# Optimization experiments

Measured on AMD Instinct MI355X. Metric: run time of the kernel, lower is better.

## Reference

```python
import jax, jax.numpy as jnp
import numpy as np

# Dimensions
N = 100000      # nodes
E = 500000      # edges
D_IN = 128      # in_channels
H, C = 2, 64    # heads, out_channels per head (out_channels=128)
T = 128         # time_enc.out_channels
MSG = 128       # msg_dim
EDGE_DIM = MSG + T  # 256
SCALE = 1.0 / np.sqrt(C)


def setup_inputs() -> dict:
    key = jax.random.key(0)
    ks = jax.random.split(key, 16)
    s = 0.05
    x = jax.random.normal(ks[0], (N, D_IN), dtype=jnp.float32)
    last_update = jax.random.uniform(ks[1], (N,), dtype=jnp.float32)
    edge_index = jax.random.randint(ks[2], (2, E), 0, N, dtype=jnp.int64)
    t = jax.random.uniform(ks[3], (E,), dtype=jnp.float32) + 1.0  # event times >= last_update typically
    msg = jax.random.normal(ks[4], (E, MSG), dtype=jnp.float32)
    # TimeEncoder: cos(Linear(1, T))
    time_w = jax.random.normal(ks[5], (T, 1), dtype=jnp.float32) * s
    time_b = jax.random.normal(ks[6], (T,), dtype=jnp.float32) * s
    # TransformerConv linear layers (PyG defaults: q/k/v with bias, edge without, skip with bias)
    Wq = jax.random.normal(ks[7], (D_IN, H * C), dtype=jnp.float32) * s
    bq = jnp.zeros((H * C,), dtype=jnp.float32)
    Wk = jax.random.normal(ks[8], (D_IN, H * C), dtype=jnp.float32) * s
    bk = jnp.zeros((H * C,), dtype=jnp.float32)
    Wv = jax.random.normal(ks[9], (D_IN, H * C), dtype=jnp.float32) * s
    bv = jnp.zeros((H * C,), dtype=jnp.float32)
    We = jax.random.normal(ks[10], (EDGE_DIM, H * C), dtype=jnp.float32) * s
    Wskip = jax.random.normal(ks[11], (D_IN, H * C), dtype=jnp.float32) * s
    bskip = jnp.zeros((H * C,), dtype=jnp.float32)
    return dict(x=x, last_update=last_update, edge_index=edge_index, t=t, msg=msg,
                time_w=time_w, time_b=time_b, Wq=Wq, bq=bq, Wk=Wk, bk=bk,
                Wv=Wv, bv=bv, We=We, Wskip=Wskip, bskip=bskip)


def reference(x, last_update, edge_index, t, msg, time_w, time_b,
              Wq, bq, Wk, bk, Wv, bv, We, Wskip, bskip):
    src, dst = edge_index[0], edge_index[1]
    # relative time encoding: cos(Linear(1, T)(rel_t))
    rel_t = t - last_update[src]                                   # [E]
    rel_t_enc = jnp.cos(rel_t[:, None] * time_w[:, 0][None, :] + time_b)  # [E, T]
    edge_attr = jnp.concatenate([rel_t_enc, msg], axis=-1)         # [E, EDGE_DIM]

    # TransformerConv (heads=H, per-head dim C, eval mode so no dropout)
    q = (x @ Wq + bq).reshape(N, H, C)
    k = (x @ Wk + bk).reshape(N, H, C)
    v = (x @ Wv + bv).reshape(N, H, C)
    e = (edge_attr @ We).reshape(E, H, C)

    k_j = k[src] + e                                               # [E, H, C]
    logits = jnp.sum(q[dst] * k_j, axis=-1) * SCALE                # [E, H]

    # segment softmax over destination nodes
    m = jax.ops.segment_max(logits, dst, num_segments=N)           # [N, H]
    p = jnp.exp(logits - m[dst])
    denom = jax.ops.segment_sum(p, dst, num_segments=N)
    alpha = p / (denom[dst] + 1e-16)                               # [E, H]

    msgs = (v[src] + e) * alpha[..., None]                         # [E, H, C]
    out = jax.ops.segment_sum(msgs, dst, num_segments=N).reshape(N, H * C)
    # root/skip connection
    return out + x @ Wskip + bskip
```

## Files before the change

### kernel.cpp

```cpp
#include <hip/hip_runtime.h>
#include <hip/hip_bf16.h>
#include <math.h>


#define SCALE_ATTN 0.125f
#define SCAN_CHUNK 512

typedef __attribute__((ext_vector_type(8))) short bf16x8;
typedef __attribute__((ext_vector_type(4))) float f32x4;

union AFrag { bf16x8 v; unsigned int w[4]; unsigned short u[8]; };

__device__ __forceinline__ unsigned short f2bf(float f) {
    __hip_bfloat16 h = __float2bfloat16(f);
    unsigned short u;
    __builtin_memcpy(&u, &h, 2);
    return u;
}
__device__ __forceinline__ unsigned int f2bf2(float lo, float hi) {
    __hip_bfloat162 h2 = __float22bfloat162_rn(float2{lo, hi});
    unsigned int u;
    __builtin_memcpy(&u, &h2, 4);
    return u;
}
__device__ __forceinline__ float bf2f(unsigned int lo16) {
    return __uint_as_float(lo16 << 16);
}
__device__ __forceinline__ void unpack8(uint4 u, float* f) {
    f[0] = bf2f(u.x & 0xffffu); f[1] = bf2f(u.x >> 16);
    f[2] = bf2f(u.y & 0xffffu); f[3] = bf2f(u.y >> 16);
    f[4] = bf2f(u.z & 0xffffu); f[5] = bf2f(u.z >> 16);
    f[6] = bf2f(u.w & 0xffffu); f[7] = bf2f(u.w >> 16);
}
__device__ __forceinline__ bf16x8 pack2(float4 a, float4 b) {
    AFrag f;
    f.w[0] = f2bf2(a.x, a.y);
    f.w[1] = f2bf2(a.z, a.w);
    f.w[2] = f2bf2(b.x, b.y);
    f.w[3] = f2bf2(b.z, b.w);
    return f.v;
}

__global__ __launch_bounds__(256) void k_zero(int4* __restrict__ p, int n4)
{
    const int i = blockIdx.x * 256 + threadIdx.x;
    if (i < n4) p[i] = make_int4(0, 0, 0, 0);
}

__global__ __launch_bounds__(512, 4) void k_node_mfma(
    const float4* __restrict__ x4,
    const float* __restrict__ Wq, const float* __restrict__ Wk,
    const float* __restrict__ Wv, const float* __restrict__ Ws,
    const float* __restrict__ bq, const float* __restrict__ bk,
    const float* __restrict__ bv, const float* __restrict__ bs,
    unsigned short* __restrict__ qb, unsigned short* __restrict__ kb,
    unsigned short* __restrict__ vb, unsigned short* __restrict__ skb,
    int N, int numTiles)
{
    __shared__ __align__(16) unsigned short sX[32 * 128];
    const int tid = threadIdx.x;
    const int w = tid >> 6, l = tid & 63;
    const int l15 = l & 15, lg = l >> 4;
    const int mat = w >> 1;
    const int colbase = (w & 1) * 64;

    const float* Wm = (mat == 0) ? Wq : (mat == 1) ? Wk : (mat == 2) ? Wv : Ws;
    const float* bm = (mat == 0) ? bq : (mat == 1) ? bk : (mat == 2) ? bv : bs;
    unsigned short* dst = (mat == 0) ? qb : (mat == 1) ? kb : (mat == 2) ? vb : skb;

    bf16x8 Bf[4][4];
    float bias[4];
    #pragma unroll
    for (int nt = 0; nt < 4; ++nt) {
        const int col = colbase + nt * 16 + l15;
        bias[nt] = bm[col];
        #pragma unroll
        for (int ks = 0; ks < 4; ++ks) {
            AFrag f;
            #pragma unroll
            for (int j = 0; j < 4; ++j)
                f.w[j] = f2bf2(Wm[(ks * 32 + lg * 8 + j * 2) * 128 + col],
                               Wm[(ks * 32 + lg * 8 + j * 2 + 1) * 128 + col]);
            Bf[ks][nt] = f.v;
        }
    }

    for (int tile = blockIdx.x; tile < numTiles; tile += gridDim.x) {
        {
            const int e = tid >> 4, k8 = tid & 15;
            const int row = min(tile * 32 + e, N - 1);
            const float4 a0 = x4[(size_t)row * 32 + k8 * 2];
            const float4 a1 = x4[(size_t)row * 32 + k8 * 2 + 1];
            const int byteoff = (e * 256 + k8 * 16) ^ ((e & 7) << 4);
            *(bf16x8*)((char*)sX + byteoff) = pack2(a0, a1);
        }
        __syncthreads();

        f32x4 acc[2][4];
        #pragma unroll
        for (int m = 0; m < 2; ++m)
            #pragma unroll
            for (int nt = 0; nt < 4; ++nt) acc[m][nt] = (f32x4)(0.f);

        #pragma unroll
        for (int m = 0; m < 2; ++m) {
            const int lrow = m * 16 + l15;
            #pragma unroll
            for (int ks = 0; ks < 4; ++ks) {
                const int byteoff = (lrow * 256 + ks * 64 + lg * 16) ^ ((lrow & 7) << 4);
                const bf16x8 a = *(const bf16x8*)((const char*)sX + byteoff);
                #pragma unroll
                for (int nt = 0; nt < 4; ++nt)
                    acc[m][nt] = __builtin_amdgcn_mfma_f32_16x16x32_bf16(a, Bf[ks][nt], acc[m][nt], 0, 0, 0);
            }
        }

        #pragma unroll
        for (int m = 0; m < 2; ++m) {
            #pragma unroll
            for (int nt = 0; nt < 4; ++nt) {
                const int col = colbase + nt * 16 + l15;
                #pragma unroll
                for (int r = 0; r < 4; ++r) {
                    const int node = tile * 32 + m * 16 + lg * 4 + r;
                    if (node < N)
                        dst[(size_t)node * 128 + col] = f2bf(acc[m][nt][r] + bias[nt]);
                }
            }
        }
        __syncthreads();
    }
}

__global__ __launch_bounds__(256, 2) void k_edge_mfma(
    const float4* __restrict__ msg4,
    const float* __restrict__ relo,
    const float4* __restrict__ tw4, const float4* __restrict__ tb4,
    const float* __restrict__ We,
    unsigned short* __restrict__ ebuf, int E, int numTiles)
{
    __shared__ __align__(16) unsigned short sWe[128 * 256];
    __shared__ __align__(16) unsigned short sMsg[64 * 128];
    const int tid = threadIdx.x;
    const int w = tid >> 6, l = tid & 63;
    const int l15 = l & 15, lg = l >> 4;
    const int ch = w & 1;
    const int mp = w >> 1;

    for (int c = tid; c < 4096; c += 256) {
        const int n = c >> 5, k0 = (c & 31) << 3;
        AFrag af;
        #pragma unroll
        for (int j = 0; j < 4; ++j)
            af.w[j] = f2bf2(We[(k0 + j * 2) * 128 + n], We[(k0 + j * 2 + 1) * 128 + n]);
        const int byteoff = ((n << 9) + (k0 << 1)) ^ ((n & 7) << 4);
        *(bf16x8*)((char*)sWe + byteoff) = af.v;
    }
    __syncthreads();

    for (int tile = blockIdx.x; tile < numTiles; tile += gridDim.x) {
        const int ebase = tile * 64;

        #pragma unroll
        for (int i = 0; i < 4; ++i) {
            const int U = tid + i * 256;
            const int e = U >> 4, u = U & 15;
            const int er = min(ebase + e, E - 1);
            const float4 a0 = msg4[(size_t)er * 32 + u * 2];
            const float4 a1 = msg4[(size_t)er * 32 + u * 2 + 1];
            const int byteoff = (e << 8) + ((u ^ (e & 7)) << 4);
            *(bf16x8*)((char*)sMsg + byteoff) = pack2(a0, a1);
        }
        __syncthreads();

        const int r0 = mp * 32 + l15;
        const int r1 = r0 + 16;
        const float rel0 = relo[min(ebase + r0, E - 1)];
        const float rel1 = relo[min(ebase + r1, E - 1)];

        f32x4 acc0[4], acc1[4];
        #pragma unroll
        for (int i = 0; i < 4; ++i) { acc0[i] = (f32x4)(0.f); acc1[i] = (f32x4)(0.f); }

        #pragma unroll
        for (int kk = 0; kk < 4; ++kk) {
            const int kbase = (kk << 5) + (lg << 3);

            const float4 tww = tw4[kbase >> 2];
            const float4 tw2 = tw4[(kbase >> 2) + 1];
            const float4 tbb = tb4[kbase >> 2];
            const float4 tb2 = tb4[(kbase >> 2) + 1];
            AFrag a0, a1;
            a0.w[0] = f2bf2(__cosf(fmaf(rel0, tww.x, tbb.x)),
                            __cosf(fmaf(rel0, tww.y, tbb.y)));
            a0.w[1] = f2bf2(__cosf(fmaf(rel0, tww.z, tbb.z)),
                            __cosf(fmaf(rel0, tww.w, tbb.w)));
            a0.w[2] = f2bf2(__cosf(fmaf(rel0, tw2.x, tb2.x)),
                            __cosf(fmaf(rel0, tw2.y, tb2.y)));
            a0.w[3] = f2bf2(__cosf(fmaf(rel0, tw2.z, tb2.z)),
                            __cosf(fmaf(rel0, tw2.w, tb2.w)));
            a1.w[0] = f2bf2(__cosf(fmaf(rel1, tww.x, tbb.x)),
                            __cosf(fmaf(rel1, tww.y, tbb.y)));
            a1.w[1] = f2bf2(__cosf(fmaf(rel1, tww.z, tbb.z)),
                            __cosf(fmaf(rel1, tww.w, tbb.w)));
            a1.w[2] = f2bf2(__cosf(fmaf(rel1, tw2.x, tb2.x)),
                            __cosf(fmaf(rel1, tw2.y, tb2.y)));
            a1.w[3] = f2bf2(__cosf(fmaf(rel1, tw2.z, tb2.z)),
                            __cosf(fmaf(rel1, tw2.w, tb2.w)));

            const int mu = (kk << 2) + lg;
            const bf16x8 am0 = *(const bf16x8*)((const char*)sMsg +
                                 ((r0 << 8) + ((mu ^ (r0 & 7)) << 4)));
            const bf16x8 am1 = *(const bf16x8*)((const char*)sMsg +
                                 ((r1 << 8) + ((mu ^ (r1 & 7)) << 4)));

            #pragma unroll
            for (int nt = 0; nt < 4; ++nt) {
                const int nrow = ch * 64 + nt * 16 + l15;
                const int swz = (nrow & 7) << 4;
                const bf16x8 bC = *(const bf16x8*)((const char*)sWe +
                                   (((nrow << 9) + (kbase << 1)) ^ swz));
                acc0[nt] = __builtin_amdgcn_mfma_f32_16x16x32_bf16(a0.v, bC, acc0[nt], 0, 0, 0);
                acc1[nt] = __builtin_amdgcn_mfma_f32_16x16x32_bf16(a1.v, bC, acc1[nt], 0, 0, 0);
                const bf16x8 bM = *(const bf16x8*)((const char*)sWe +
                                   (((nrow << 9) + ((128 + kbase) << 1)) ^ swz));
                acc0[nt] = __builtin_amdgcn_mfma_f32_16x16x32_bf16(am0, bM, acc0[nt], 0, 0, 0);
                acc1[nt] = __builtin_amdgcn_mfma_f32_16x16x32_bf16(am1, bM, acc1[nt], 0, 0, 0);
            }
        }

        #pragma unroll
        for (int nt = 0; nt < 4; ++nt) {
            const int col = ch * 64 + nt * 16 + l15;
            #pragma unroll
            for (int r = 0; r < 4; ++r) {
                const int e0 = ebase + mp * 32 + (lg << 2) + r;
                const int e1 = e0 + 16;
                if (e0 < E) ebuf[(size_t)e0 * 128 + col] = f2bf(acc0[nt][r]);
                if (e1 < E) ebuf[(size_t)e1 * 128 + col] = f2bf(acc1[nt][r]);
            }
        }
        __syncthreads();
    }
}

__global__ __launch_bounds__(256) void k_hist(
    const int* __restrict__ ei, int* __restrict__ counts, int E)
{
    int i = blockIdx.x * 256 + threadIdx.x;
    if (i < E) atomicAdd(&counts[ei[E + i]], 1);
}

__global__ __launch_bounds__(256) void k_scan_partial(
    const int* __restrict__ counts, int* __restrict__ partial, int N)
{
    const int base = blockIdx.x * SCAN_CHUNK;
    int v = 0;
    for (int i = threadIdx.x; i < SCAN_CHUNK; i += 256) {
        const int idx = base + i;
        if (idx < N) v += counts[idx];
    }
    __shared__ int red[4];
    #pragma unroll
    for (int off = 1; off < 64; off <<= 1) v += __shfl_xor(v, off);
    if ((threadIdx.x & 63) == 0) red[threadIdx.x >> 6] = v;
    __syncthreads();
    if (threadIdx.x == 0) partial[blockIdx.x] = red[0] + red[1] + red[2] + red[3];
}

__global__ __launch_bounds__(256) void k_scan_base(
    const int* __restrict__ partial, int* __restrict__ base, int nb)
{
    __shared__ int tmp[256];
    const int v = (threadIdx.x < nb) ? partial[threadIdx.x] : 0;
    tmp[threadIdx.x] = v;
    __syncthreads();
    for (int off = 1; off < 256; off <<= 1) {
        const int add = (threadIdx.x >= off) ? tmp[threadIdx.x - off] : 0;
        __syncthreads();
        tmp[threadIdx.x] += add;
        __syncthreads();
    }
    if (threadIdx.x < nb) base[threadIdx.x] = tmp[threadIdx.x] - v;
}

__global__ __launch_bounds__(256) void k_scan_final(
    const int* __restrict__ counts, const int* __restrict__ base,
    int* __restrict__ rowptr, int* __restrict__ cursor, int N)
{
    const int i0 = blockIdx.x * SCAN_CHUNK;
    __shared__ int tmp[256];
    const int ia = i0 + threadIdx.x * 2, ib = ia + 1;
    const int v0 = (ia < N) ? counts[ia] : 0;
    const int v1 = (ib < N) ? counts[ib] : 0;
    const int s = v0 + v1;
    tmp[threadIdx.x] = s;
    __syncthreads();
    for (int off = 1; off < 256; off <<= 1) {
        const int add = (threadIdx.x >= off) ? tmp[threadIdx.x - off] : 0;
        __syncthreads();
        tmp[threadIdx.x] += add;
        __syncthreads();
    }
    const int excl = tmp[threadIdx.x] - s + base[blockIdx.x];
    if (ia < N) { rowptr[ia] = excl;      cursor[ia] = excl; }
    if (ib < N) { rowptr[ib] = excl + v0; cursor[ib] = excl + v0; }
}

__global__ __launch_bounds__(256) void k_fill(
    const int* __restrict__ ei, const float* __restrict__ t,
    const float* __restrict__ lu, int* __restrict__ cursor,
    int* __restrict__ perm, int* __restrict__ srcp,
    float* __restrict__ relo, int E)
{
    int i = blockIdx.x * 256 + threadIdx.x;
    if (i < E) {
        const int s = ei[i];
        const int d = ei[E + i];
        const int pos = atomicAdd(&cursor[d], 1);
        perm[pos] = i;
        srcp[pos] = s;
        relo[i] = t[i] - lu[s];
    }
}

__global__ __launch_bounds__(256) void k_agg(
    const int* __restrict__ srcp, const int* __restrict__ perm,
    const int* __restrict__ rowptr, const int* __restrict__ counts,
    const uint4* __restrict__ qb4, const uint4* __restrict__ kb4,
    const uint4* __restrict__ vb4, const uint4* __restrict__ eb4,
    const uint4* __restrict__ skb4, float4* __restrict__ out4, int N)
{
    const int tid = threadIdx.x;
    const int l = tid & 63;
    const int half = l >> 5;
    const int l5 = l & 31;
    const int eg = l5 >> 4;
    const int s16 = l & 15;
    const int d = blockIdx.x * 8 + ((tid >> 6) << 1) + half;
    if (d >= N) return;
    const int start = rowptr[d];
    const int deg = counts[d];

    float qf[8];
    unpack8(qb4[(size_t)d * 16 + s16], qf);
    float accf[8] = {0.f, 0.f, 0.f, 0.f, 0.f, 0.f, 0.f, 0.f};
    float denom = 0.f;

    for (int cbase = 0; cbase < deg; cbase += 32) {
        const int clen = min(deg - cbase, 32);
        int mySrc = 0, myEid = 0;
        if (l5 < clen) {
            mySrc = srcp[start + cbase + l5];
            myEid = perm[start + cbase + l5];
        }

        #pragma unroll 2
        for (int i = 0; i < clen; i += 2) {
            const int off = i + eg;
            const bool valid = off < clen;
            const int offc = valid ? off : 0;
            const int src = __shfl(mySrc, (half << 5) + offc);
            const int eid = __shfl(myEid, (half << 5) + offc);
            if (valid) {
                float kf[8], ef[8], vf[8];
                unpack8(kb4[(size_t)src * 16 + s16], kf);
                unpack8(eb4[(size_t)eid * 16 + s16], ef);
                unpack8(vb4[(size_t)src * 16 + s16], vf);
                float s = 0.f;
                #pragma unroll
                for (int j = 0; j < 8; ++j) s = fmaf(qf[j], kf[j] + ef[j], s);
                s += __shfl_xor(s, 1);
                s += __shfl_xor(s, 2);
                s += __shfl_xor(s, 4);
                const float p = __expf(s * SCALE_ATTN);
                denom += p;
                #pragma unroll
                for (int j = 0; j < 8; ++j) accf[j] = fmaf(p, vf[j] + ef[j], accf[j]);
            }
        }
    }
    #pragma unroll
    for (int j = 0; j < 8; ++j) accf[j] += __shfl_xor(accf[j], 16);
    denom += __shfl_xor(denom, 16);

    if (l5 < 16) {
        const float inv = 1.f / (denom + 1e-16f);
        float sk[8];
        unpack8(skb4[(size_t)d * 16 + s16], sk);
        float4* o = out4 + (size_t)d * 32 + s16 * 2;
        o[0] = make_float4(fmaf(accf[0], inv, sk[0]), fmaf(accf[1], inv, sk[1]),
                           fmaf(accf[2], inv, sk[2]), fmaf(accf[3], inv, sk[3]));
        o[1] = make_float4(fmaf(accf[4], inv, sk[4]), fmaf(accf[5], inv, sk[5]),
                           fmaf(accf[6], inv, sk[6]), fmaf(accf[7], inv, sk[7]));
    }
}

extern "C" void kernel_launch(void* const* d_in, const int* in_sizes, int n_in,
                              void* d_out, int out_size, void* d_ws, size_t ws_size,
                              hipStream_t stream)
{
    const float* x   = (const float*)d_in[0];
    const float* lu  = (const float*)d_in[1];
    const int*   ei  = (const int*)d_in[2];
    const float* t   = (const float*)d_in[3];
    const float* msg = (const float*)d_in[4];
    const float* tw  = (const float*)d_in[5];
    const float* tb  = (const float*)d_in[6];
    const float* Wq  = (const float*)d_in[7];
    const float* bq  = (const float*)d_in[8];
    const float* Wk  = (const float*)d_in[9];
    const float* bk  = (const float*)d_in[10];
    const float* Wv  = (const float*)d_in[11];
    const float* bv  = (const float*)d_in[12];
    const float* We  = (const float*)d_in[13];
    const float* Wsk = (const float*)d_in[14];
    const float* bsk = (const float*)d_in[15];

    const int N = in_sizes[1];
    const int E = in_sizes[3];
    float* out = (float*)d_out;

    char* ws = (char*)d_ws;
    unsigned short* qb  = (unsigned short*)ws;  ws += (size_t)N * 128 * sizeof(unsigned short);
    unsigned short* kb  = (unsigned short*)ws;  ws += (size_t)N * 128 * sizeof(unsigned short);
    unsigned short* vb  = (unsigned short*)ws;  ws += (size_t)N * 128 * sizeof(unsigned short);
    unsigned short* skb = (unsigned short*)ws;  ws += (size_t)N * 128 * sizeof(unsigned short);
    unsigned short* eb  = (unsigned short*)ws;  ws += (size_t)E * 128 * sizeof(unsigned short);
    int*   counts  = (int*)ws;   ws += (size_t)N * sizeof(int);
    int*   rowptr  = (int*)ws;   ws += (size_t)N * sizeof(int);
    int*   cursor  = (int*)ws;   ws += (size_t)N * sizeof(int);
    int*   perm    = (int*)ws;   ws += (size_t)E * sizeof(int);
    int*   srcp    = (int*)ws;   ws += (size_t)E * sizeof(int);
    float* relo    = (float*)ws; ws += (size_t)E * sizeof(float);
    int*   partial = (int*)ws;   ws += 512 * sizeof(int);
    int*   baseArr = (int*)ws;   ws += 512 * sizeof(int);

    const int nScan = (N + SCAN_CHUNK - 1) / SCAN_CHUNK;

    const int n4 = (N + 3) / 4;
    k_zero<<<(n4 + 255) / 256, 256, 0, stream>>>((int4*)counts, n4);

    k_hist<<<(E + 255) / 256, 256, 0, stream>>>(ei, counts, E);
    k_scan_partial<<<nScan, 256, 0, stream>>>(counts, partial, N);
    k_scan_base<<<1, 256, 0, stream>>>(partial, baseArr, nScan);
    k_scan_final<<<nScan, 256, 0, stream>>>(counts, baseArr, rowptr, cursor, N);
    k_fill<<<(E + 255) / 256, 256, 0, stream>>>(ei, t, lu, cursor, perm, srcp, relo, E);

    const int nTN = (N + 31) / 32;
    k_node_mfma<<<min(nTN, 1024), 512, 0, stream>>>(
        (const float4*)x, Wq, Wk, Wv, Wsk, bq, bk, bv, bsk,
        qb, kb, vb, skb, N, nTN);

    const int nTE = (E + 63) / 64;
    k_edge_mfma<<<min(nTE, 512), 256, 0, stream>>>(
        (const float4*)msg, relo,
        (const float4*)tw, (const float4*)tb, We, eb, E, nTE);

    k_agg<<<(N + 7) / 8, 256, 0, stream>>>(
        srcp, perm, rowptr, counts,
        (const uint4*)qb, (const uint4*)kb, (const uint4*)vb, (const uint4*)eb,
        (const uint4*)skb, (float4*)out, N);
}
```

Before: 314.8 us.

## Stage time-encoding and msg into one shared A tile, use 512-thread edge blocks

The edge GEMM kernel now computes each cosine time-encoding value once per edge and writes it into shared memory next to the bf16 message, forming a 64x256 A tile. Before, each wave recomputed cosines in registers for its own rows. The MFMA loop becomes a uniform 8-step K loop with one accumulator set per wave. Blocks grow to 512 threads (8 waves, one block per CU) and the grid drops to 256 blocks. This removes redundant cosine work and simplifies the inner loop, at the cost of more LDS per block and lower block-level occupancy.

```diff
diff --git a/kernel.cpp b/kernel.cpp
--- a/kernel.cpp
+++ b/kernel.cpp
@@ -132,7 +132,7 @@
     }
 }
 
-__global__ __launch_bounds__(256, 2) void k_edge_mfma(
+__global__ __launch_bounds__(512, 1) void k_edge_mfma(
     const float4* __restrict__ msg4,
     const float* __restrict__ relo,
     const float4* __restrict__ tw4, const float4* __restrict__ tb4,
@@ -140,14 +140,16 @@
     unsigned short* __restrict__ ebuf, int E, int numTiles)
 {
     __shared__ __align__(16) unsigned short sWe[128 * 256];
-    __shared__ __align__(16) unsigned short sMsg[64 * 128];
+    __shared__ __align__(16) unsigned short sA[64 * 256];
     const int tid = threadIdx.x;
     const int w = tid >> 6, l = tid & 63;
     const int l15 = l & 15, lg = l >> 4;
-    const int ch = w & 1;
-    const int mp = w >> 1;
-
-    for (int c = tid; c < 4096; c += 256) {
+    const int mp = w & 3;
+    const int ch = w >> 2;
+    const int u = tid & 31;
+    const int e0 = tid >> 5;
+
+    for (int c = tid; c < 4096; c += 512) {
         const int n = c >> 5, k0 = (c & 31) << 3;
         AFrag af;
         #pragma unroll
@@ -163,69 +165,52 @@
 
         #pragma unroll
         for (int i = 0; i < 4; ++i) {
-            const int U = tid + i * 256;
-            const int e = U >> 4, u = U & 15;
+            const int e = e0 + i * 16;
             const int er = min(ebase + e, E - 1);
-            const float4 a0 = msg4[(size_t)er * 32 + u * 2];
-            const float4 a1 = msg4[(size_t)er * 32 + u * 2 + 1];
-            const int byteoff = (e << 8) + ((u ^ (e & 7)) << 4);
-            *(bf16x8*)((char*)sMsg + byteoff) = pack2(a0, a1);
-        }
-        __syncthreads();
-
-        const int r0 = mp * 32 + l15;
-        const int r1 = r0 + 16;
-        const float rel0 = relo[min(ebase + r0, E - 1)];
-        const float rel1 = relo[min(ebase + r1, E - 1)];
-
-        f32x4 acc0[4], acc1[4];
-        #pragma unroll
-        for (int i = 0; i < 4; ++i) { acc0[i] = (f32x4)(0.f); acc1[i] = (f32x4)(0.f); }
-
-        #pragma unroll
-        for (int kk = 0; kk < 4; ++kk) {
-            const int kbase = (kk << 5) + (lg << 3);
-
-            const float4 tww = tw4[kbase >> 2];
-            const float4 tw2 = tw4[(kbase >> 2) + 1];
-            const float4 tbb = tb4[kbase >> 2];
-            const float4 tb2 = tb4[(kbase >> 2) + 1];
-            AFrag a0, a1;
-            a0.w[0] = f2bf2(__cosf(fmaf(rel0, tww.x, tbb.x)),
-                            __cosf(fmaf(rel0, tww.y, tbb.y)));
-            a0.w[1] = f2bf2(__cosf(fmaf(rel0, tww.z, tbb.z)),
-                            __cosf(fmaf(rel0, tww.w, tbb.w)));
-            a0.w[2] = f2bf2(__cosf(fmaf(rel0, tw2.x, tb2.x)),
-                            __cosf(fmaf(rel0, tw2.y, tb2.y)));
-            a0.w[3] = f2bf2(__cosf(fmaf(rel0, tw2.z, tb2.z)),
-                            __cosf(fmaf(rel0, tw2.w, tb2.w)));
-            a1.w[0] = f2bf2(__cosf(fmaf(rel1, tww.x, tbb.x)),
-                            __cosf(fmaf(rel1, tww.y, tbb.y)));
-            a1.w[1] = f2bf2(__cosf(fmaf(rel1, tww.z, tbb.z)),
-                            __cosf(fmaf(rel1, tww.w, tbb.w)));
-            a1.w[2] = f2bf2(__cosf(fmaf(rel1, tw2.x, tb2.x)),
-                            __cosf(fmaf(rel1, tw2.y, tb2.y)));
-            a1.w[3] = f2bf2(__cosf(fmaf(rel1, tw2.z, tb2.z)),
-                            __cosf(fmaf(rel1, tw2.w, tb2.w)));
-
-            const int mu = (kk << 2) + lg;
-            const bf16x8 am0 = *(const bf16x8*)((const char*)sMsg +
-                                 ((r0 << 8) + ((mu ^ (r0 & 7)) << 4)));
-            const bf16x8 am1 = *(const bf16x8*)((const char*)sMsg +
-                                 ((r1 << 8) + ((mu ^ (r1 & 7)) << 4)));
-
+            bf16x8 val;
+            if (u < 16) {
+                const float rel = relo[er];
+                const float4 tww = tw4[u * 2];
+                const float4 tw2 = tw4[u * 2 + 1];
+                const float4 tbb = tb4[u * 2];
+                const float4 tb2 = tb4[u * 2 + 1];
+                AFrag c;
+                c.w[0] = f2bf2(__cosf(fmaf(rel, tww.x, tbb.x)),
+                               __cosf(fmaf(rel, tww.y, tbb.y)));
+                c.w[1] = f2bf2(__cosf(fmaf(rel, tww.z, tbb.z)),
+                               __cosf(fmaf(rel, tww.w, tbb.w)));
+                c.w[2] = f2bf2(__cosf(fmaf(rel, tw2.x, tb2.x)),
+                               __cosf(fmaf(rel, tw2.y, tb2.y)));
+                c.w[3] = f2bf2(__cosf(fmaf(rel, tw2.z, tb2.z)),
+                               __cosf(fmaf(rel, tw2.w, tb2.w)));
+                val = c.v;
+            } else {
+                const float4 a0 = msg4[(size_t)er * 32 + (u - 16) * 2];
+                const float4 a1 = msg4[(size_t)er * 32 + (u - 16) * 2 + 1];
+                val = pack2(a0, a1);
+            }
+            const int byteoff = (e << 9) + ((u ^ (e & 7)) << 4);
+            *(bf16x8*)((char*)sA + byteoff) = val;
+        }
+        __syncthreads();
+
+        f32x4 acc[4];
+        #pragma unroll
+        for (int nt = 0; nt < 4; ++nt) acc[nt] = (f32x4)(0.f);
+
+        const int row = mp * 16 + l15;
+        #pragma unroll
+        for (int ks = 0; ks < 8; ++ks) {
+            const int ur = ks * 4 + lg;
+            const bf16x8 a = *(const bf16x8*)((const char*)sA +
+                               ((row << 9) + ((ur ^ (row & 7)) << 4)));
             #pragma unroll
             for (int nt = 0; nt < 4; ++nt) {
                 const int nrow = ch * 64 + nt * 16 + l15;
                 const int swz = (nrow & 7) << 4;
-                const bf16x8 bC = *(const bf16x8*)((const char*)sWe +
-                                   (((nrow << 9) + (kbase << 1)) ^ swz));
-                acc0[nt] = __builtin_amdgcn_mfma_f32_16x16x32_bf16(a0.v, bC, acc0[nt], 0, 0, 0);
-                acc1[nt] = __builtin_amdgcn_mfma_f32_16x16x32_bf16(a1.v, bC, acc1[nt], 0, 0, 0);
-                const bf16x8 bM = *(const bf16x8*)((const char*)sWe +
-                                   (((nrow << 9) + ((128 + kbase) << 1)) ^ swz));
-                acc0[nt] = __builtin_amdgcn_mfma_f32_16x16x32_bf16(am0, bM, acc0[nt], 0, 0, 0);
-                acc1[nt] = __builtin_amdgcn_mfma_f32_16x16x32_bf16(am1, bM, acc1[nt], 0, 0, 0);
+                const bf16x8 b = *(const bf16x8*)((const char*)sWe +
+                                   (((nrow << 9) + (ks * 64 + lg * 16)) ^ swz));
+                acc[nt] = __builtin_amdgcn_mfma_f32_16x16x32_bf16(a, b, acc[nt], 0, 0, 0);
             }
         }
 
@@ -234,10 +219,8 @@
             const int col = ch * 64 + nt * 16 + l15;
             #pragma unroll
             for (int r = 0; r < 4; ++r) {
-                const int e0 = ebase + mp * 32 + (lg << 2) + r;
-                const int e1 = e0 + 16;
-                if (e0 < E) ebuf[(size_t)e0 * 128 + col] = f2bf(acc0[nt][r]);
-                if (e1 < E) ebuf[(size_t)e1 * 128 + col] = f2bf(acc1[nt][r]);
+                const int er = ebase + mp * 16 + (lg << 2) + r;
+                if (er < E) ebuf[(size_t)er * 128 + col] = f2bf(acc[nt][r]);
             }
         }
         __syncthreads();
@@ -453,7 +436,7 @@
         qb, kb, vb, skb, N, nTN);
 
     const int nTE = (E + 63) / 64;
-    k_edge_mfma<<<min(nTE, 512), 256, 0, stream>>>(
+    k_edge_mfma<<<min(nTE, 256), 512, 0, stream>>>(
         (const float4*)msg, relo,
         (const float4*)tw, (const float4*)tb, We, eb, E, nTE);
 
```

After: 390.1 us. 23.9% more time.
